# Kernel tuning notes

Measured on AMD Instinct MI355X. Metric: run time of the kernel, lower is better.

## Reference

```python
import jax, jax.numpy as jnp
import numpy as np

# Dimensions
B, V, K, H = 64, 2048, 128, 128   # graphs, verts/graph, eigenvectors, h_dim
N = B * V                          # total verts
E = 1048576                        # total neighbor entries
CF = 47                            # chem feat dim = 15 + 2*num_gdf (num_gdf=16)
L = 3                              # num_prop_layers
EPS = 1e-5                         # BatchNorm eps
PROP_SCALE = 1.0                   # propagation_time_scale


def setup_inputs() -> dict:
    key = jax.random.key(0)
    ks = iter(jax.random.split(key, 48))
    nk = lambda: next(ks)
    nrm = lambda shape, s: jax.random.normal(nk(), shape, jnp.float32) * s

    chem_feats = jax.random.normal(nk(), (E, CF), jnp.float32)
    nbr_vid = jax.random.randint(nk(), (E,), 0, N)
    # eigs layout per graph: row 0 = eigen_vals (K,), rows 1..V = eigen_vecs (V,K),
    # rows V+1..2V = eigen_vecs_inv stored as (V,K) (transposed at use site)
    eig_vals = jax.random.uniform(nk(), (B, 1, K), jnp.float32) * 2.0
    vecs = jax.random.normal(nk(), (B, V, K), jnp.float32) / np.sqrt(V)
    vecs_inv = jax.random.normal(nk(), (B, V, K), jnp.float32) / np.sqrt(V)
    eigs = jnp.concatenate([eig_vals, vecs, vecs_inv], axis=1)  # [B, 1+2V, K]

    inp = dict(chem_feats=chem_feats, nbr_vid=nbr_vid, eigs=eigs)
    # chem_mlp params
    inp.update(w1=nrm((CF, H), 0.1), b1=jnp.zeros(H), g1=jnp.ones(H), be1=jnp.zeros(H),
               w2=nrm((H, 2 * H), 0.1), b2=jnp.zeros(2 * H), g2=jnp.ones(2 * H), be2=jnp.zeros(2 * H))
    # propagation layers (stacked across L)
    inp.update(prop_time=jnp.abs(jax.random.normal(nk(), (L, H), jnp.float32)) + 0.1,
               pw1=nrm((L, 2 * H, H), 0.05), pb1=jnp.zeros((L, H)), pg1=jnp.ones((L, H)), pbe1=jnp.zeros((L, H)),
               pw2=nrm((L, H, H), 0.05), pb2=jnp.zeros((L, H)), pg2=jnp.ones((L, H)), pbe2=jnp.zeros((L, H)))
    # out_mlp params
    inp.update(wo1=nrm((H, H), 0.1), bo1=jnp.zeros(H), go1=jnp.ones(H), beo1=jnp.zeros(H),
               wo2=nrm((H, 1), 0.1), bo2=jnp.zeros(1))
    return inp


def _bn(x, g, b):
    # BatchNorm1d in training mode: biased batch stats
    m = jnp.mean(x, axis=0)
    v = jnp.var(x, axis=0)
    return g * (x - m) * jax.lax.rsqrt(v + EPS) + b


def reference(chem_feats, nbr_vid, eigs, w1, b1, g1, be1, w2, b2, g2, be2,
              prop_time, pw1, pb1, pg1, pbe1, pw2, pb2, pg2, pbe2,
              wo1, bo1, go1, beo1, wo2, bo2):
    # --- FeatExtractor ---
    h_chem = _bn(chem_feats @ w1 + b1, g1, be1)
    h_chem = jax.nn.silu(h_chem)
    h_chem = _bn(h_chem @ w2 + b2, g2, be2)             # [E, 2H]
    nbr_filter, nbr_core = h_chem[:, :H], h_chem[:, H:]
    msg = jax.nn.sigmoid(nbr_filter) * jax.nn.softplus(nbr_core)
    h = jax.ops.segment_sum(msg, nbr_vid, num_segments=N)  # [N, H]

    # --- eigen decomposition pieces (uniform per-graph sizes -> batched) ---
    eigen_vals = eigs[:, 0, :]                      # [B, K]
    evecs = eigs[:, 1:1 + V, :]                     # [B, V, K]
    evecs_inv = jnp.swapaxes(eigs[:, 1 + V:, :], 1, 2)  # [B, K, V]

    # --- PropagationLayers ---
    for l in range(L):
        pt = prop_time[l]
        # torch clamps .data in-place under no_grad, then uses it: value clamped, grad passes
        pt = pt + jax.lax.stop_gradient(jnp.clip(pt, 1e-6) - pt)
        time = PROP_SCALE * pt                      # [H]
        hb = h.reshape(B, V, H)
        h_spec = jnp.einsum('bkv,bvh->bkh', evecs_inv, hb)
        coeff = jnp.exp(-eigen_vals[:, :, None] * time[None, None, :])  # [B, K, H]
        h_prop = jnp.einsum('bvk,bkh->bvh', evecs, coeff * h_spec).reshape(N, H)
        z = jnp.concatenate([h, h_prop], axis=-1)   # [N, 2H]
        z = jax.nn.silu(_bn(z @ pw1[l] + pb1[l], pg1[l], pbe1[l]))
        z = _bn(z @ pw2[l] + pb2[l], pg2[l], pbe2[l])
        h = h + z

    # --- out_mlp + per-graph mean ---
    out = jax.nn.silu(_bn(h @ wo1 + bo1, go1, beo1)) @ wo2 + bo2  # [N, 1]
    return out.reshape(B, V, 1).mean(axis=1)        # [B, 1]
```

## Files before the change

kernel.cpp:

```cpp
#include <hip/hip_runtime.h>
#include <hip/hip_bf16.h>
#include <math.h>

#define E_N 1048576
#define CF 47
#define H 128
#define H2 256
#define B_N 64
#define V_N 2048
#define K_N 128
#define N_N 131072
#define EPSf 1e-5f
#define EVS 132

typedef __attribute__((ext_vector_type(8))) short short8;
typedef __attribute__((ext_vector_type(4))) float f32x4;

__device__ __forceinline__ float bf2f(unsigned int u16) {
  union { float f; unsigned int i; } x; x.i = u16 << 16; return x.f;
}
__device__ __forceinline__ unsigned int f2bf_rne(float f) {
  unsigned int u = __float_as_uint(f);
  return (u + 0x7fffu + ((u >> 16) & 1u)) >> 16;
}
__device__ __forceinline__ unsigned int packbf2(float lo, float hi) {
  return f2bf_rne(lo) | (f2bf_rne(hi) << 16);
}
__device__ __forceinline__ float frcp_(float x) { return __builtin_amdgcn_rcpf(x); }
__device__ __forceinline__ float sigmf_(float x) { return frcp_(1.f + __expf(-x)); }
__device__ __forceinline__ float siluf_(float x) { return x * sigmf_(x); }
__device__ __forceinline__ float splusf_(float x) {
  return (x > 15.f) ? x : __logf(1.f + __expf(x));
}

extern "C" __global__ __launch_bounds__(256) void k_gemm1_stats(
    const float* __restrict__ chem, const float* __restrict__ w1,
    const float* __restrict__ b1, __hip_bfloat16* __restrict__ x1,
    float* __restrict__ sum1, float* __restrict__ ssq1)
{
  __shared__ float w1s[CF * H];
  __shared__ float csh[8 * CF];
  __shared__ float red[256];
  const int tid = threadIdx.x;
  for (int i = tid; i < CF * H; i += 256) w1s[i] = w1[i];
  const int c = tid & 127, half = tid >> 7;
  const float bc = b1[c];
  const int rowbase = blockIdx.x * 128;
  float s = 0.f, sq = 0.f;
  for (int chunk = 0; chunk < 16; ++chunk) {
    const int rb = rowbase + chunk * 8;
    __syncthreads();
    for (int i = tid; i < 8 * CF; i += 256) csh[i] = chem[(size_t)rb * CF + i];
    __syncthreads();
    const int roff = half * 4;
    float a0 = bc, a1 = bc, a2 = bc, a3 = bc;
    for (int k = 0; k < CF; ++k) {
      const float w = w1s[k * H + c];
      a0 += csh[(roff + 0) * CF + k] * w;
      a1 += csh[(roff + 1) * CF + k] * w;
      a2 += csh[(roff + 2) * CF + k] * w;
      a3 += csh[(roff + 3) * CF + k] * w;
    }
    const size_t r = (size_t)(rb + roff) * H + c;
    x1[r]         = __float2bfloat16(a0);
    x1[r + H]     = __float2bfloat16(a1);
    x1[r + 2 * H] = __float2bfloat16(a2);
    x1[r + 3 * H] = __float2bfloat16(a3);
    s  += a0 + a1 + a2 + a3;
    sq += a0 * a0 + a1 * a1 + a2 * a2 + a3 * a3;
  }
  red[tid] = s; __syncthreads();
  if (half == 0) atomicAdd(&sum1[c], red[c] + red[c + 128]);
  __syncthreads();
  red[tid] = sq; __syncthreads();
  if (half == 0) atomicAdd(&ssq1[c], red[c] + red[c + 128]);
}

extern "C" __global__ void k_bnfin(const float* __restrict__ sum, const float* __restrict__ ssq,
    const float* __restrict__ g, const float* __restrict__ be, float invn,
    float* __restrict__ sc, float* __restrict__ sh)
{
  const int c = threadIdx.x;
  const float m = sum[c] * invn;
  const float v = ssq[c] * invn - m * m;
  const float s = g[c] * rsqrtf(v + EPSf);
  sc[c] = s;
  sh[c] = be[c] - m * s;
}

extern "C" __global__ __launch_bounds__(256) void k_a1_gram(
    __hip_bfloat16* __restrict__ x1, const float* __restrict__ sc1,
    const float* __restrict__ sh1, float* __restrict__ asum, float* __restrict__ G)
{
  __shared__ float as[128 * 128];
  __shared__ float scs[128], shs[128];
  const int tid = threadIdx.x;
  if (tid < 128) { scs[tid] = sc1[tid]; shs[tid] = sh1[tid]; }
  const int i0 = (tid >> 4) * 8, j0 = (tid & 15) * 8;
  float g[8][8];
  #pragma unroll
  for (int a = 0; a < 8; ++a)
    #pragma unroll
    for (int b = 0; b < 8; ++b) g[a][b] = 0.f;
  float colsum = 0.f;
  for (int tile = blockIdx.x; tile < E_N / 128; tile += gridDim.x) {
    __syncthreads();
    const size_t base = (size_t)tile * (128 * 128);
    for (int i = tid * 8; i < 128 * 128; i += 256 * 8) {
      const uint4 pk = *(const uint4*)(x1 + base + i);
      const int col = i & 127;
      float v[8];
      v[0] = bf2f(pk.x & 0xffff); v[1] = bf2f(pk.x >> 16);
      v[2] = bf2f(pk.y & 0xffff); v[3] = bf2f(pk.y >> 16);
      v[4] = bf2f(pk.z & 0xffff); v[5] = bf2f(pk.z >> 16);
      v[6] = bf2f(pk.w & 0xffff); v[7] = bf2f(pk.w >> 16);
      #pragma unroll
      for (int j = 0; j < 8; ++j) {
        v[j] = siluf_(v[j] * scs[col + j] + shs[col + j]);
        as[i + j] = v[j];
      }
      uint4 o;
      o.x = packbf2(v[0], v[1]); o.y = packbf2(v[2], v[3]);
      o.z = packbf2(v[4], v[5]); o.w = packbf2(v[6], v[7]);
      *(uint4*)(x1 + base + i) = o;
    }
    __syncthreads();
    for (int r = 0; r < 128; ++r) {
      const float4 xa = *(const float4*)&as[r * 128 + i0];
      const float4 xb = *(const float4*)&as[r * 128 + i0 + 4];
      const float4 ya = *(const float4*)&as[r * 128 + j0];
      const float4 yb = *(const float4*)&as[r * 128 + j0 + 4];
      const float ax[8] = {xa.x, xa.y, xa.z, xa.w, xb.x, xb.y, xb.z, xb.w};
      const float ay[8] = {ya.x, ya.y, ya.z, ya.w, yb.x, yb.y, yb.z, yb.w};
      #pragma unroll
      for (int a = 0; a < 8; ++a)
        #pragma unroll
        for (int b = 0; b < 8; ++b) g[a][b] += ax[a] * ay[b];
    }
    if (tid < 128) {
      for (int r = 0; r < 128; ++r) colsum += as[r * 128 + tid];
    }
  }
  #pragma unroll
  for (int a = 0; a < 8; ++a)
    #pragma unroll
    for (int b = 0; b < 8; ++b) atomicAdd(&G[(i0 + a) * 128 + (j0 + b)], g[a][b]);
  if (tid < 128) atomicAdd(&asum[tid], colsum);
}

extern "C" __global__ __launch_bounds__(256) void k_bn2fin(
    const float* __restrict__ asum, const float* __restrict__ Gm,
    const float* __restrict__ w2, const float* __restrict__ g2,
    const float* __restrict__ be2, float* __restrict__ sc2, float* __restrict__ sh2)
{
  __shared__ float Gs[128 * 128];
  __shared__ float w2s[128 * 128];
  __shared__ float mus[128];
  __shared__ float red[512];
  const int tid = threadIdx.x;
  const int jbase = blockIdx.x * 128;
  for (int i = tid; i < 128 * 128; i += 256) {
    Gs[i] = Gm[i];
    w2s[i] = w2[(i >> 7) * H2 + jbase + (i & 127)];
  }
  if (tid < 128) mus[tid] = asum[tid] * (1.f / (float)E_N);
  __syncthreads();
  const int jj = tid & 127, ih = tid >> 7;
  float m1 = 0.f, q = 0.f;
  for (int i = ih * 64; i < ih * 64 + 64; ++i) {
    const float wi = w2s[i * 128 + jj];
    m1 += mus[i] * wi;
    float si = 0.f;
    #pragma unroll 4
    for (int k = 0; k < 128; ++k) si += Gs[i * 128 + k] * w2s[k * 128 + jj];
    q += wi * si;
  }
  red[tid] = m1; red[256 + tid] = q;
  __syncthreads();
  if (ih == 0) {
    const float m1t = red[jj] + red[jj + 128];
    const float qt  = red[256 + jj] + red[256 + jj + 128];
    const float var = qt * (1.f / (float)E_N) - m1t * m1t;
    const float s = g2[jbase + jj] * rsqrtf(var + EPSf);
    sc2[jbase + jj] = s;
    sh2[jbase + jj] = be2[jbase + jj] - m1t * s;
  }
}

extern "C" __global__ __launch_bounds__(256) void k_hist(
    const int* __restrict__ nbr, int* __restrict__ cnt)
{
  const int e = blockIdx.x * 256 + threadIdx.x;
  atomicAdd(&cnt[nbr[e]], 1);
}

extern "C" __global__ __launch_bounds__(256) void k_scan1(
    const int* __restrict__ cnt, int* __restrict__ bsum)
{
  __shared__ int rs[256];
  const int tid = threadIdx.x, b = blockIdx.x;
  const int4 c = *(const int4*)&cnt[b * 1024 + tid * 4];
  rs[tid] = c.x + c.y + c.z + c.w;
  __syncthreads();
  for (int o = 128; o > 0; o >>= 1) {
    if (tid < o) rs[tid] += rs[tid + o];
    __syncthreads();
  }
  if (tid == 0) bsum[b] = rs[0];
}

extern "C" __global__ void k_scan2(const int* __restrict__ bsum, int* __restrict__ bpre)
{
  __shared__ int bs[128];
  const int tid = threadIdx.x;
  bs[tid] = bsum[tid];
  __syncthreads();
  int p = 0;
  for (int i = 0; i < tid; ++i) p += bs[i];
  bpre[tid] = p;
}

extern "C" __global__ __launch_bounds__(256) void k_scan3(
    const int* __restrict__ cnt, const int* __restrict__ bpre,
    int* __restrict__ cursor, int* __restrict__ rowptr)
{
  __shared__ int tsum[256];
  const int tid = threadIdx.x, b = blockIdx.x;
  const int4 c = *(const int4*)&cnt[b * 1024 + tid * 4];
  const int t1 = c.x, t2 = c.x + c.y, t3 = c.x + c.y + c.z, tot = t3 + c.w;
  tsum[tid] = tot;
  __syncthreads();
  for (int o = 1; o < 256; o <<= 1) {
    const int add = (tid >= o) ? tsum[tid - o] : 0;
    __syncthreads();
    tsum[tid] += add;
    __syncthreads();
  }
  const int excl = (tid == 0) ? 0 : tsum[tid - 1];
  const int base = bpre[b] + excl;
  int4 o4;
  o4.x = base; o4.y = base + t1; o4.z = base + t2; o4.w = base + t3;
  *(int4*)&cursor[b * 1024 + tid * 4] = o4;
  *(int4*)&rowptr[b * 1024 + tid * 4] = o4;
}

extern "C" __global__ __launch_bounds__(256) void k_scatteridx(
    const int* __restrict__ nbr, int* __restrict__ cursor,
    int* __restrict__ sorted_eid)
{
  const int e = blockIdx.x * 256 + threadIdx.x;
  const int v = nbr[e];
  const int pos = atomicAdd(&cursor[v], 1);
  sorted_eid[pos] = e;
}

extern "C" __global__ void k_packB(const float* __restrict__ w2, __hip_bfloat16* __restrict__ Bpack)
{
  const int i = blockIdx.x * 256 + threadIdx.x;
  const int j = i & 7, L = (i >> 3) & 63, s = (i >> 9) & 3, t = i >> 11;
  const int k = s * 32 + (L >> 4) * 8 + j;
  const int n = t * 16 + (L & 15);
  Bpack[i] = __float2bfloat16(w2[k * H2 + n]);
}

extern "C" __global__ __launch_bounds__(256) void k_msg(
    const __hip_bfloat16* __restrict__ a1, const int* __restrict__ sorted_eid,
    const __hip_bfloat16* __restrict__ Bpack,
    const float* __restrict__ sc2, const float* __restrict__ sh2,
    __hip_bfloat16* __restrict__ msgbuf, const int eoff)
{
  __shared__ __hip_bfloat16 As[128 * 136];
  __shared__ int eidsh[128];
  __shared__ float sc2s[256], sh2s[256];
  const int tid = threadIdx.x;
  const int s0 = blockIdx.x * 128;
  if (tid < 128) eidsh[tid] = sorted_eid[eoff + s0 + tid];
  sc2s[tid] = sc2[tid]; sh2s[tid] = sh2[tid];
  __syncthreads();
  for (int i = tid; i < 128 * 16; i += 256) {
    const int r = i >> 4, cc = (i & 15) * 8;
    *(uint4*)&As[r * 136 + cc] = *(const uint4*)(a1 + (size_t)eidsh[r] * H + cc);
  }
  __syncthreads();
  const int w = tid >> 6, L = tid & 63, lm = L & 15, q = L >> 4;
  const int m0 = w * 32, m1 = w * 32 + 16;
  f32x4 acc0[16], acc1[16];
  #pragma unroll
  for (int t = 0; t < 16; ++t) { acc0[t] = (f32x4){0.f,0.f,0.f,0.f}; acc1[t] = (f32x4){0.f,0.f,0.f,0.f}; }
  const short8* bp = (const short8*)Bpack;
  #pragma unroll
  for (int s = 0; s < 4; ++s) {
    const short8 af0 = *(const short8*)&As[(m0 + lm) * 136 + s * 32 + q * 8];
    const short8 af1 = *(const short8*)&As[(m1 + lm) * 136 + s * 32 + q * 8];
    #pragma unroll
    for (int t = 0; t < 16; ++t) {
      const short8 bf = bp[(t * 4 + s) * 64 + L];
      acc0[t] = __builtin_amdgcn_mfma_f32_16x16x32_bf16(af0, bf, acc0[t], 0, 0, 0);
      acc1[t] = __builtin_amdgcn_mfma_f32_16x16x32_bf16(af1, bf, acc1[t], 0, 0, 0);
    }
  }
  #pragma unroll
  for (int t = 0; t < 8; ++t) {
    const int cF = t * 16 + lm;
    const float scF = sc2s[cF], shF = sh2s[cF];
    const float scC = sc2s[128 + cF], shC = sh2s[128 + cF];
    #pragma unroll
    for (int r = 0; r < 4; ++r) {
      const int row0 = m0 + q * 4 + r, row1 = m1 + q * 4 + r;
      const float f0 = acc0[t][r] * scF + shF;
      const float g0 = acc0[t + 8][r] * scC + shC;
      const float f1 = acc1[t][r] * scF + shF;
      const float g1 = acc1[t + 8][r] * scC + shC;
      As[row0 * 136 + cF] = __hip_bfloat16();
      ((unsigned short*)As)[row0 * 136 + cF] = (unsigned short)f2bf_rne(sigmf_(f0) * splusf_(g0));
      ((unsigned short*)As)[row1 * 136 + cF] = (unsigned short)f2bf_rne(sigmf_(f1) * splusf_(g1));
    }
  }
  __syncthreads();
  for (int i = tid; i < 128 * 16; i += 256) {
    const int r = i >> 4, cc = (i & 15) * 8;
    *(uint4*)(msgbuf + ((size_t)(s0 + r)) * H + cc) = *(const uint4*)&As[r * 136 + cc];
  }
}

extern "C" __global__ __launch_bounds__(256) void k_segsum(
    const __hip_bfloat16* __restrict__ msgbuf, const int* __restrict__ rowptr,
    const int* __restrict__ cnt, float* __restrict__ h,
    const int w0, const int w1, const int mode)
{
  __shared__ float redA[256], redB[256];
  const int tid = threadIdx.x;
  const int c2 = (tid & 63) * 2;
  const int j  = tid >> 6;
  const int n0 = blockIdx.x * 16;
  for (int g = 0; g < 16; ++g) {
    const int n = n0 + g;
    const int s = rowptr[n], e = s + cnt[n];
    const int lo = max(s, w0), hi = min(e, w1);
    float s0 = 0.f, s1 = 0.f;
    for (int r = lo + j; r < hi; r += 4) {
      const unsigned int pk = *(const unsigned int*)(msgbuf + ((size_t)(r - w0)) * H + c2);
      s0 += bf2f(pk & 0xffff);
      s1 += bf2f(pk >> 16);
    }
    redA[tid] = s0; redB[tid] = s1;
    __syncthreads();
    if (j == 0) {
      const int t = tid;
      const float t0 = redA[t] + redA[t + 64] + redA[t + 128] + redA[t + 192];
      const float t1 = redB[t] + redB[t + 64] + redB[t + 128] + redB[t + 192];
      float* hp = h + (size_t)n * H + c2;
      if (mode == 0) { hp[0] = t0; hp[1] = t1; }
      else           { hp[0] += t0; hp[1] += t1; }
    }
    __syncthreads();
  }
}

extern "C" __global__ __launch_bounds__(256) void k_spec(
    const float* __restrict__ eigs, const float* __restrict__ h,
    const float* __restrict__ prop_time, int l, float* __restrict__ CS)
{
  __shared__ float Ash[64 * 32];
  __shared__ float Hsh[64 * 128];
  const int tid = threadIdx.x;
  const int b = blockIdx.x >> 2;
  const int kbase = (blockIdx.x & 3) * 32;
  const int k0 = (tid >> 5) * 4;
  const int c0 = (tid & 31) * 4;
  const size_t ebase = (size_t)b * (4097 * 128);
  float acc[4][4] = {};
  for (int vb = 0; vb < V_N; vb += 64) {
    __syncthreads();
    for (int i = tid * 4; i < 64 * 32; i += 1024) {
      const int vv = i >> 5, kk = i & 31;
      *(float4*)&Ash[i] = *(const float4*)&eigs[ebase + (size_t)(2049 + vb + vv) * 128 + kbase + kk];
    }
    for (int i = tid * 4; i < 64 * 128; i += 1024)
      *(float4*)&Hsh[i] = *(const float4*)&h[((size_t)b * V_N + vb) * 128 + i];
    __syncthreads();
    for (int vv = 0; vv < 64; ++vv) {
      const float4 av = *(const float4*)&Ash[vv * 32 + k0];
      const float4 hv = *(const float4*)&Hsh[vv * 128 + c0];
      const float aa[4] = {av.x, av.y, av.z, av.w};
      const float hh[4] = {hv.x, hv.y, hv.z, hv.w};
      #pragma unroll
      for (int a = 0; a < 4; ++a)
        #pragma unroll
        for (int j = 0; j < 4; ++j) acc[a][j] += aa[a] * hh[j];
    }
  }
  #pragma unroll
  for (int a = 0; a < 4; ++a) {
    const float ev = eigs[ebase + kbase + k0 + a];
    #pragma unroll
    for (int j = 0; j < 4; ++j) {
      const float tm = fmaxf(prop_time[l * H + c0 + j], 1e-6f);
      CS[((size_t)b * K_N + kbase + k0 + a) * H + c0 + j] = __expf(-ev * tm) * acc[a][j];
    }
  }
}

extern "C" __global__ __launch_bounds__(256) void k_hprop(
    const float* __restrict__ eigs, const float* __restrict__ CS,
    float* __restrict__ hprop)
{
  __shared__ float EvT[32 * EVS];
  __shared__ float CSsh[32 * 128];
  const int tid = threadIdx.x;
  const int b = blockIdx.x >> 4;
  const int vbase = (blockIdx.x & 15) * 128;
  const int v0 = (tid >> 4) * 8;
  const int c0 = (tid & 15) * 8;
  const size_t ebase = (size_t)b * (4097 * 128);
  float acc[8][8] = {};
  for (int kb = 0; kb < K_N; kb += 32) {
    __syncthreads();
    for (int i = tid; i < 128 * 32; i += 256) {
      const int vv = i >> 5, kk = i & 31;
      EvT[kk * EVS + vv] = eigs[ebase + (size_t)(1 + vbase + vv) * 128 + kb + kk];
    }
    for (int i = tid * 4; i < 32 * 128; i += 1024)
      *(float4*)&CSsh[i] = *(const float4*)&CS[((size_t)b * K_N + kb) * 128 + i];
    __syncthreads();
    for (int kk = 0; kk < 32; ++kk) {
      const float4 ea = *(const float4*)&EvT[kk * EVS + v0];
      const float4 eb = *(const float4*)&EvT[kk * EVS + v0 + 4];
      const float4 ca = *(const float4*)&CSsh[kk * 128 + c0];
      const float4 cb = *(const float4*)&CSsh[kk * 128 + c0 + 4];
      const float ee[8] = {ea.x, ea.y, ea.z, ea.w, eb.x, eb.y, eb.z, eb.w};
      const float cc[8] = {ca.x, ca.y, ca.z, ca.w, cb.x, cb.y, cb.z, cb.w};
      #pragma unroll
      for (int a = 0; a < 8; ++a)
        #pragma unroll
        for (int j = 0; j < 8; ++j) acc[a][j] += ee[a] * cc[j];
    }
  }
  #pragma unroll
  for (int a = 0; a < 8; ++a) {
    const size_t row = ((size_t)b * V_N + vbase + v0 + a) * H;
    #pragma unroll
    for (int j = 0; j < 8; j += 4) {
      float4 o;
      o.x = acc[a][j]; o.y = acc[a][j+1]; o.z = acc[a][j+2]; o.w = acc[a][j+3];
      *(float4*)&hprop[row + c0 + j] = o;
    }
  }
}

extern "C" __global__ __launch_bounds__(256) void k_gemm(
    const float* __restrict__ A0, const float* __restrict__ A1,
    const float* __restrict__ W, const float* __restrict__ bias,
    const float* __restrict__ preSc, const float* __restrict__ preSh,
    const int preop, const int KcA, float* __restrict__ out,
    float* __restrict__ sum, float* __restrict__ ssq)
{
  __shared__ float AT[32 * EVS];
  __shared__ float Ws[32 * 128];
  __shared__ float cs[128], cq[128];
  const int tid = threadIdx.x;
  const int rbase = blockIdx.x * 128;
  const int r0 = (tid >> 4) * 8;
  const int c0 = (tid & 15) * 8;
  float acc[8][8] = {};
  for (int kb = 0; kb < KcA; kb += 32) {
    const float* Asrc = (kb < 128) ? A0 : A1;
    const int kloc = kb & 127;
    __syncthreads();
    for (int i = tid; i < 128 * 32; i += 256) {
      const int rr = i >> 5, kk = i & 31;
      float v = Asrc[((size_t)rbase + rr) * H + kloc + kk];
      if (preop) {
        v = v * preSc[kloc + kk] + preSh[kloc + kk];
        v = siluf_(v);
      }
      AT[kk * EVS + rr] = v;
    }
    for (int i = tid * 4; i < 32 * 128; i += 1024)
      *(float4*)&Ws[i] = *(const float4*)&W[(size_t)kb * 128 + i];
    __syncthreads();
    for (int kk = 0; kk < 32; ++kk) {
      const float4 aa4 = *(const float4*)&AT[kk * EVS + r0];
      const float4 ab4 = *(const float4*)&AT[kk * EVS + r0 + 4];
      const float4 wa4 = *(const float4*)&Ws[kk * 128 + c0];
      const float4 wb4 = *(const float4*)&Ws[kk * 128 + c0 + 4];
      const float ar[8] = {aa4.x, aa4.y, aa4.z, aa4.w, ab4.x, ab4.y, ab4.z, ab4.w};
      const float wr[8] = {wa4.x, wa4.y, wa4.z, wa4.w, wb4.x, wb4.y, wb4.z, wb4.w};
      #pragma unroll
      for (int a = 0; a < 8; ++a)
        #pragma unroll
        for (int j = 0; j < 8; ++j) acc[a][j] += ar[a] * wr[j];
    }
  }
  if (tid < 128) { cs[tid] = 0.f; cq[tid] = 0.f; }
  __syncthreads();
  float s8[8] = {}, q8[8] = {};
  #pragma unroll
  for (int a = 0; a < 8; ++a) {
    const size_t row = ((size_t)rbase + r0 + a) * H;
    float val[8];
    #pragma unroll
    for (int j = 0; j < 8; ++j) {
      val[j] = acc[a][j] + bias[c0 + j];
      s8[j] += val[j];
      q8[j] += val[j] * val[j];
    }
    #pragma unroll
    for (int j = 0; j < 8; j += 4) {
      float4 o; o.x = val[j]; o.y = val[j+1]; o.z = val[j+2]; o.w = val[j+3];
      *(float4*)&out[row + c0 + j] = o;
    }
  }
  #pragma unroll
  for (int j = 0; j < 8; ++j) {
    atomicAdd(&cs[c0 + j], s8[j]);
    atomicAdd(&cq[c0 + j], q8[j]);
  }
  __syncthreads();
  if (tid < 128) {
    atomicAdd(&sum[tid], cs[tid]);
    atomicAdd(&ssq[tid], cq[tid]);
  }
}

extern "C" __global__ __launch_bounds__(256) void k_hupd(
    float* __restrict__ h, const float* __restrict__ tb,
    const float* __restrict__ sc, const float* __restrict__ sh)
{
  const int i4 = blockIdx.x * 256 + threadIdx.x;
  const size_t base = (size_t)i4 * 4;
  const int c = (int)(base & 127);
  float4 t = *(const float4*)&tb[base];
  float4 hh = *(const float4*)&h[base];
  hh.x += sc[c+0]*t.x + sh[c+0];
  hh.y += sc[c+1]*t.y + sh[c+1];
  hh.z += sc[c+2]*t.z + sh[c+2];
  hh.w += sc[c+3]*t.w + sh[c+3];
  *(float4*)&h[base] = hh;
}

extern "C" __global__ __launch_bounds__(256) void k_head(
    const float* __restrict__ ta, const float* __restrict__ sc,
    const float* __restrict__ sh, const float* __restrict__ wo2,
    const float* __restrict__ bo2, float* __restrict__ out)
{
  __shared__ float w2s[128], scs[128], shs[128];
  __shared__ float wred[4];
  const int tid = threadIdx.x;
  if (tid < 128) { w2s[tid] = wo2[tid]; scs[tid] = sc[tid]; shs[tid] = sh[tid]; }
  __syncthreads();
  const int b = blockIdx.x;
  const int wave = tid >> 6, lane = tid & 63;
  const int j = lane * 2;
  const float w0 = w2s[j], w1 = w2s[j+1];
  const float s0 = scs[j], s1 = scs[j+1], t0 = shs[j], t1 = shs[j+1];
  float p = 0.f;
  for (int v = wave; v < V_N; v += 4) {
    const float2 xv = *(const float2*)&ta[((size_t)b * V_N + v) * H + j];
    float x0 = xv.x * s0 + t0; x0 = siluf_(x0);
    float x1 = xv.y * s1 + t1; x1 = siluf_(x1);
    p += x0 * w0 + x1 * w1;
  }
  #pragma unroll
  for (int off = 32; off > 0; off >>= 1) p += __shfl_down(p, off);
  if (lane == 0) wred[wave] = p;
  __syncthreads();
  if (tid == 0) out[b] = (wred[0] + wred[1] + wred[2] + wred[3]) * (1.f / V_N) + bo2[0];
}

extern "C" void kernel_launch(void* const* d_in, const int* in_sizes, int n_in,
                              void* d_out, int out_size, void* d_ws, size_t ws_size,
                              hipStream_t stream) {
  (void)in_sizes; (void)n_in; (void)out_size;
  const float* chem = (const float*)d_in[0];
  const int*   nbr  = (const int*)d_in[1];
  const float* eigs = (const float*)d_in[2];
  const float* w1   = (const float*)d_in[3];
  const float* b1   = (const float*)d_in[4];
  const float* g1   = (const float*)d_in[5];
  const float* be1  = (const float*)d_in[6];
  const float* w2   = (const float*)d_in[7];
  const float* b2   = (const float*)d_in[8];  (void)b2;
  const float* g2   = (const float*)d_in[9];
  const float* be2  = (const float*)d_in[10];
  const float* prop_time = (const float*)d_in[11];
  const float* pw1  = (const float*)d_in[12];
  const float* pb1  = (const float*)d_in[13];
  const float* pg1  = (const float*)d_in[14];
  const float* pbe1 = (const float*)d_in[15];
  const float* pw2  = (const float*)d_in[16];
  const float* pb2  = (const float*)d_in[17];
  const float* pg2  = (const float*)d_in[18];
  const float* pbe2 = (const float*)d_in[19];
  const float* wo1  = (const float*)d_in[20];
  const float* bo1  = (const float*)d_in[21];
  const float* go1  = (const float*)d_in[22];
  const float* beo1 = (const float*)d_in[23];
  const float* wo2  = (const float*)d_in[24];
  const float* bo2  = (const float*)d_in[25];

  float* ws = (float*)d_ws;
  float* h     = ws;
  float* hprop = h + (size_t)N_N * H;
  float* ta    = hprop + (size_t)N_N * H;
  float* CS    = ta + (size_t)N_N * H;
  float* acc   = CS + (size_t)B_N * K_N * H;
  float* sum1 = acc,        *ssq1 = acc + 128;
  float* sc1  = acc + 256,  *sh1  = acc + 384;
  float* asum = acc + 512;
  float* G    = acc + 640;
  float* sc2  = acc + 17024, *sh2 = acc + 17280;
  float* statS = acc + 17536;
  float* scA = acc + 19456, *shA = acc + 19584;
  float* scB = acc + 19712, *shB = acc + 19840;
  __hip_bfloat16* x1 = (__hip_bfloat16*)(acc + 19968);

  char* p = (char*)x1 + (size_t)E_N * H * 2;
  int* cnt        = (int*)p;  p += (size_t)N_N * 4;
  int* cursor     = (int*)p;  p += (size_t)N_N * 4;
  int* rowptr     = (int*)p;  p += (size_t)N_N * 4;
  int* bsum       = (int*)p;  p += 512;
  int* bpre       = (int*)p;  p += 512;
  int* sorted_eid = (int*)p;  p += (size_t)E_N * 4;
  __hip_bfloat16* Bpack = (__hip_bfloat16*)p;  p += 65536;

  const size_t req = (size_t)(p - (char*)d_ws);
  if (ws_size < req) return;

  __hip_bfloat16* msgbuf = (__hip_bfloat16*)hprop;

  hipMemsetAsync(acc, 0, 19456 * sizeof(float), stream);
  hipMemsetAsync(cnt, 0, (size_t)N_N * sizeof(int), stream);

  k_gemm1_stats<<<E_N / 128, 256, 0, stream>>>(chem, w1, b1, x1, sum1, ssq1);
  k_bnfin<<<1, 128, 0, stream>>>(sum1, ssq1, g1, be1, 1.f / (float)E_N, sc1, sh1);
  k_a1_gram<<<512, 256, 0, stream>>>(x1, sc1, sh1, asum, G);
  k_bn2fin<<<2, 256, 0, stream>>>(asum, G, w2, g2, be2, sc2, sh2);

  k_packB<<<128, 256, 0, stream>>>(w2, Bpack);
  k_hist<<<E_N / 256, 256, 0, stream>>>(nbr, cnt);
  k_scan1<<<128, 256, 0, stream>>>(cnt, bsum);
  k_scan2<<<1, 128, 0, stream>>>(bsum, bpre);
  k_scan3<<<128, 256, 0, stream>>>(cnt, bpre, cursor, rowptr);
  k_scatteridx<<<E_N / 256, 256, 0, stream>>>(nbr, cursor, sorted_eid);

  for (int half = 0; half < 2; ++half) {
    const int w0 = half * (E_N / 2), w1e = w0 + E_N / 2;
    k_msg<<<(E_N / 2) / 128, 256, 0, stream>>>(x1, sorted_eid, Bpack, sc2, sh2, msgbuf, w0);
    k_segsum<<<N_N / 16, 256, 0, stream>>>(msgbuf, rowptr, cnt, h, w0, w1e, half);
  }

  float* tb = hprop;
  for (int l = 0; l < 3; ++l) {
    k_spec<<<B_N * 4, 256, 0, stream>>>(eigs, h, prop_time, l, CS);
    k_hprop<<<B_N * 16, 256, 0, stream>>>(eigs, CS, hprop);
    k_gemm<<<N_N / 128, 256, 0, stream>>>(h, hprop, pw1 + (size_t)l * H2 * H, pb1 + l * H,
                                          nullptr, nullptr, 0, H2, ta,
                                          statS + (2 * l) * 256, statS + (2 * l) * 256 + 128);
    k_bnfin<<<1, 128, 0, stream>>>(statS + (2 * l) * 256, statS + (2 * l) * 256 + 128,
                                   pg1 + l * H, pbe1 + l * H, 1.f / (float)N_N, scA, shA);
    k_gemm<<<N_N / 128, 256, 0, stream>>>(ta, nullptr, pw2 + (size_t)l * H * H, pb2 + l * H,
                                          scA, shA, 1, H, tb,
                                          statS + (2 * l + 1) * 256, statS + (2 * l + 1) * 256 + 128);
    k_bnfin<<<1, 128, 0, stream>>>(statS + (2 * l + 1) * 256, statS + (2 * l + 1) * 256 + 128,
                                   pg2 + l * H, pbe2 + l * H, 1.f / (float)N_N, scB, shB);
    k_hupd<<<N_N * H / 1024, 256, 0, stream>>>(h, tb, scB, shB);
  }

  k_gemm<<<N_N / 128, 256, 0, stream>>>(h, nullptr, wo1, bo1, nullptr, nullptr, 0, H, ta,
                                        statS + 6 * 256, statS + 6 * 256 + 128);
  k_bnfin<<<1, 128, 0, stream>>>(statS + 6 * 256, statS + 6 * 256 + 128,
                                 go1, beo1, 1.f / (float)N_N, scA, shA);
  k_head<<<B_N, 256, 0, stream>>>(ta, scA, shA, wo2, bo2, (float*)d_out);
}
```

Measured before the change: 3.890 ms.

## Compute Gram matrix with bf16 MFMA and double-buffered LDS in a1_gram

Rewrites the Gram/column-sum kernel so the SiLU-activated tile is stored as bf16 in a transposed, swizzled LDS layout and the 128x128 Gram is accumulated with 16x16x32 bf16 MFMA instead of scalar fp32 FMAs. The next tile's global loads are issued before the current tile's MFMA work, and column sums are reduced through wave shuffles and LDS before the atomics. The grid is now assumed fixed at 512 blocks with 16 tiles each, and the Gram is built from bf16-rounded values rather than fp32, which changes precision slightly. It also drops a redundant LDS zero store in the message kernel.

```diff
diff --git a/kernel.cpp b/kernel.cpp
--- a/kernel.cpp
+++ b/kernel.cpp
@@ -92,60 +92,128 @@
     __hip_bfloat16* __restrict__ x1, const float* __restrict__ sc1,
     const float* __restrict__ sh1, float* __restrict__ asum, float* __restrict__ G)
 {
-  __shared__ float as[128 * 128];
-  __shared__ float scs[128], shs[128];
-  const int tid = threadIdx.x;
-  if (tid < 128) { scs[tid] = sc1[tid]; shs[tid] = sh1[tid]; }
-  const int i0 = (tid >> 4) * 8, j0 = (tid & 15) * 8;
-  float g[8][8];
-  #pragma unroll
-  for (int a = 0; a < 8; ++a)
-    #pragma unroll
-    for (int b = 0; b < 8; ++b) g[a][b] = 0.f;
-  float colsum = 0.f;
-  for (int tile = blockIdx.x; tile < E_N / 128; tile += gridDim.x) {
-    __syncthreads();
-    const size_t base = (size_t)tile * (128 * 128);
-    for (int i = tid * 8; i < 128 * 128; i += 256 * 8) {
-      const uint4 pk = *(const uint4*)(x1 + base + i);
-      const int col = i & 127;
-      float v[8];
-      v[0] = bf2f(pk.x & 0xffff); v[1] = bf2f(pk.x >> 16);
-      v[2] = bf2f(pk.y & 0xffff); v[3] = bf2f(pk.y >> 16);
-      v[4] = bf2f(pk.z & 0xffff); v[5] = bf2f(pk.z >> 16);
-      v[6] = bf2f(pk.w & 0xffff); v[7] = bf2f(pk.w >> 16);
-      #pragma unroll
-      for (int j = 0; j < 8; ++j) {
-        v[j] = siluf_(v[j] * scs[col + j] + shs[col + j]);
-        as[i + j] = v[j];
+  __shared__ __align__(16) unsigned short frag[2][16384];
+  const int tid = threadIdx.x;
+  const int rb = tid >> 4, u = tid & 15;
+  const int kb = rb >> 2, qw = rb & 3;
+  const int th = u >> 1;
+  const int cmb = (u & 1) * 8;
+  const int cg = u * 8;
+  const int w = tid >> 6;
+  const int lq = (tid >> 4) & 3;
+  const int cm = tid & 15;
+  const int tib = (w >> 1) * 4, tjb = (w & 1) * 4;
+
+  float scv[8], shv[8];
+  #pragma unroll
+  for (int jc = 0; jc < 8; ++jc) { scv[jc] = sc1[cg + jc]; shv[jc] = sh1[cg + jc]; }
+
+  float cs8[8] = {0.f, 0.f, 0.f, 0.f, 0.f, 0.f, 0.f, 0.f};
+  f32x4 acc[4][4];
+  #pragma unroll
+  for (int a = 0; a < 4; ++a)
+    #pragma unroll
+    for (int b = 0; b < 4; ++b) acc[a][b] = (f32x4){0.f, 0.f, 0.f, 0.f};
+
+  const int ldsbase = kb * 4096 + th * 512 + qw * 128;
+  uint4 rv[8];
+
+  auto PROCESS = [&](int bsel, size_t tb) {
+    unsigned int colw[8][4];
+    #pragma unroll
+    for (int jc = 0; jc < 8; ++jc) { colw[jc][0] = 0; colw[jc][1] = 0; colw[jc][2] = 0; colw[jc][3] = 0; }
+    #pragma unroll
+    for (int j8 = 0; j8 < 8; ++j8) {
+      const uint4 pk = rv[j8];
+      float f[8];
+      f[0] = bf2f(pk.x & 0xffff); f[1] = bf2f(pk.x >> 16);
+      f[2] = bf2f(pk.y & 0xffff); f[3] = bf2f(pk.y >> 16);
+      f[4] = bf2f(pk.z & 0xffff); f[5] = bf2f(pk.z >> 16);
+      f[6] = bf2f(pk.w & 0xffff); f[7] = bf2f(pk.w >> 16);
+      unsigned int bfv[8];
+      #pragma unroll
+      for (int jc = 0; jc < 8; ++jc) {
+        f[jc] = siluf_(f[jc] * scv[jc] + shv[jc]);
+        cs8[jc] += f[jc];
+        bfv[jc] = f2bf_rne(f[jc]);
+        colw[jc][j8 >> 1] |= bfv[jc] << (16 * (j8 & 1));
       }
       uint4 o;
-      o.x = packbf2(v[0], v[1]); o.y = packbf2(v[2], v[3]);
-      o.z = packbf2(v[4], v[5]); o.w = packbf2(v[6], v[7]);
-      *(uint4*)(x1 + base + i) = o;
-    }
-    __syncthreads();
-    for (int r = 0; r < 128; ++r) {
-      const float4 xa = *(const float4*)&as[r * 128 + i0];
-      const float4 xb = *(const float4*)&as[r * 128 + i0 + 4];
-      const float4 ya = *(const float4*)&as[r * 128 + j0];
-      const float4 yb = *(const float4*)&as[r * 128 + j0 + 4];
-      const float ax[8] = {xa.x, xa.y, xa.z, xa.w, xb.x, xb.y, xb.z, xb.w};
-      const float ay[8] = {ya.x, ya.y, ya.z, ya.w, yb.x, yb.y, yb.z, yb.w};
-      #pragma unroll
-      for (int a = 0; a < 8; ++a)
+      o.x = bfv[0] | (bfv[1] << 16); o.y = bfv[2] | (bfv[3] << 16);
+      o.z = bfv[4] | (bfv[5] << 16); o.w = bfv[6] | (bfv[7] << 16);
+      *(uint4*)(x1 + (tb + (size_t)(rb * 8 + j8)) * H + cg) = o;
+    }
+    #pragma unroll
+    for (int jc = 0; jc < 8; ++jc) {
+      const int pos = (cmb + jc + 2 * th) & 15;
+      uint4 cw;
+      cw.x = colw[jc][0]; cw.y = colw[jc][1]; cw.z = colw[jc][2]; cw.w = colw[jc][3];
+      *(uint4*)&frag[bsel][ldsbase + pos * 8] = cw;
+    }
+  };
+
+  {
+    const size_t tb = (size_t)blockIdx.x * 128;
+    #pragma unroll
+    for (int j8 = 0; j8 < 8; ++j8)
+      rv[j8] = *(const uint4*)(x1 + (tb + (size_t)(rb * 8 + j8)) * H + cg);
+    PROCESS(0, tb);
+  }
+
+  for (int k = 0; k < 16; ++k) {
+    __syncthreads();
+    const int cur = k & 1;
+    const bool hasnext = (k + 1 < 16);
+    const size_t tbn = (size_t)(blockIdx.x + (k + 1) * 512) * 128;
+    if (hasnext) {
+      #pragma unroll
+      for (int j8 = 0; j8 < 8; ++j8)
+        rv[j8] = *(const uint4*)(x1 + (tbn + (size_t)(rb * 8 + j8)) * H + cg);
+    }
+    #pragma unroll
+    for (int kk = 0; kk < 4; ++kk) {
+      short8 fa[4], fb[4];
+      #pragma unroll
+      for (int a = 0; a < 4; ++a) {
+        const int T = tib + a;
+        fa[a] = *(const short8*)&frag[cur][kk * 4096 + T * 512 + lq * 128 + ((cm + 2 * T) & 15) * 8];
+      }
+      #pragma unroll
+      for (int b = 0; b < 4; ++b) {
+        const int T = tjb + b;
+        fb[b] = *(const short8*)&frag[cur][kk * 4096 + T * 512 + lq * 128 + ((cm + 2 * T) & 15) * 8];
+      }
+      #pragma unroll
+      for (int a = 0; a < 4; ++a)
         #pragma unroll
-        for (int b = 0; b < 8; ++b) g[a][b] += ax[a] * ay[b];
-    }
-    if (tid < 128) {
-      for (int r = 0; r < 128; ++r) colsum += as[r * 128 + tid];
-    }
-  }
-  #pragma unroll
-  for (int a = 0; a < 8; ++a)
-    #pragma unroll
-    for (int b = 0; b < 8; ++b) atomicAdd(&G[(i0 + a) * 128 + (j0 + b)], g[a][b]);
-  if (tid < 128) atomicAdd(&asum[tid], colsum);
+        for (int b = 0; b < 4; ++b)
+          acc[a][b] = __builtin_amdgcn_mfma_f32_16x16x32_bf16(fa[a], fb[b], acc[a][b], 0, 0, 0);
+    }
+    if (hasnext) PROCESS(cur ^ 1, tbn);
+  }
+
+  #pragma unroll
+  for (int jc = 0; jc < 8; ++jc) {
+    cs8[jc] += __shfl_xor(cs8[jc], 16);
+    cs8[jc] += __shfl_xor(cs8[jc], 32);
+  }
+  __syncthreads();
+  float* redp = (float*)&frag[0][0];
+  if ((tid & 63) < 16) {
+    #pragma unroll
+    for (int jc = 0; jc < 8; ++jc) redp[w * 128 + (tid & 15) * 8 + jc] = cs8[jc];
+  }
+  __syncthreads();
+  if (tid < 128)
+    atomicAdd(&asum[tid], redp[tid] + redp[128 + tid] + redp[256 + tid] + redp[384 + tid]);
+
+  #pragma unroll
+  for (int a = 0; a < 4; ++a)
+    #pragma unroll
+    for (int b = 0; b < 4; ++b)
+      #pragma unroll
+      for (int r = 0; r < 4; ++r)
+        atomicAdd(&G[((tib + a) * 16 + lq * 4 + r) * 128 + (tjb + b) * 16 + cm], acc[a][b][r]);
 }
 
 extern "C" __global__ __launch_bounds__(256) void k_bn2fin(
@@ -311,7 +379,6 @@
       const float g0 = acc0[t + 8][r] * scC + shC;
       const float f1 = acc1[t][r] * scF + shF;
       const float g1 = acc1[t + 8][r] * scC + shC;
-      As[row0 * 136 + cF] = __hip_bfloat16();
       ((unsigned short*)As)[row0 * 136 + cF] = (unsigned short)f2bf_rne(sigmf_(f0) * splusf_(g0));
       ((unsigned short*)As)[row1 * 136 + cF] = (unsigned short)f2bf_rne(sigmf_(f1) * splusf_(g1));
     }
```

New measurement: 3.404 ms. 1.14x faster.
